# Kernel tuning notes

Hardware: AMD Instinct MI355X
Metric: run time of the kernel (lower is better)

The kernel has to match this reference:

```python
import jax, jax.numpy as jnp
import numpy as np

EMBED_DIM = 1024
HEAD_SIZE = 128
B, S = 8, 2048

def setup_inputs() -> dict:
    rng = jax.random.key(0)
    k1, k2, k3, k4, k5, k6 = jax.random.split(rng, 6)
    std = 1.0 / EMBED_DIM  # nn.initializers.normal(stddev=1/embed_dim)
    return {
        "key": jax.random.normal(k1, (B, S, EMBED_DIM), dtype=jnp.float32),
        "query": jax.random.normal(k2, (B, S, EMBED_DIM), dtype=jnp.float32),
        "value": jax.random.normal(k3, (B, S, EMBED_DIM), dtype=jnp.float32),
        "W_Q": jax.random.normal(k4, (EMBED_DIM, HEAD_SIZE), dtype=jnp.float32) * std,
        "W_K": jax.random.normal(k5, (EMBED_DIM, HEAD_SIZE), dtype=jnp.float32) * std,
        "W_V": jax.random.normal(k6, (EMBED_DIM, HEAD_SIZE), dtype=jnp.float32) * std,
    }

def reference(key, query, value, W_Q, W_K, W_V):
    # Parallel retention: (Q K^T * causal_mask) V
    q_proj = query @ W_Q        # (B, S, H)
    k_proj = key @ W_K          # (B, S, H)
    v_proj = value @ W_V        # (B, S, H)
    ret = jnp.einsum("bsh,bth->bst", q_proj, k_proj)  # (B, S, S)
    # full_self_retention=False -> lower-triangular (causal) mask
    decay_matrix = jnp.tril(jnp.ones((S, S), dtype=ret.dtype))
    ret = ret * decay_matrix
    return ret @ v_proj          # (B, S, H)
```

## Files before the change

### kernel.cpp

```cpp
#include <hip/hip_runtime.h>
#include <cstdint>

#define B_  8
#define S_  2048
#define E_  1024
#define H_  128
#define NC_ 16

typedef __attribute__((ext_vector_type(8))) short bf16x8;
typedef __attribute__((ext_vector_type(4))) float f32x4;

__device__ __forceinline__ short f2bf(float f){
  uint32_t u = __builtin_bit_cast(uint32_t, f);
  u = (u + 0x7fffu + ((u >> 16) & 1u)) >> 16;
  return (short)u;
}
__device__ __forceinline__ float bf2f(short s){
  uint32_t u = ((uint32_t)(uint16_t)s) << 16;
  return __builtin_bit_cast(float, u);
}
__device__ __forceinline__ void load_lds16(const void* g, void* l){
  __builtin_amdgcn_global_load_lds(
    (const __attribute__((address_space(1))) void*)g,
    (__attribute__((address_space(3))) void*)l, 16, 0, 0);
}

__global__ __launch_bounds__(256) void wt_kernel(
    const float* __restrict__ WQ, const float* __restrict__ WK,
    const float* __restrict__ WV,
    short* __restrict__ WtQ, short* __restrict__ WtK, short* __restrict__ WtV)
{
  int which = blockIdx.y;
  const float* W = which == 0 ? WQ : which == 1 ? WK : WV;
  short* Wt      = which == 0 ? WtQ : which == 1 ? WtK : WtV;
  int base = blockIdx.x * 4096;
  #pragma unroll
  for (int t = 0; t < 16; t++){
    int idx = base + t * 256 + threadIdx.x;
    int n  = idx >> 10;
    int kk = idx & 1023;
    Wt[idx] = f2bf(W[kk * H_ + n]);
  }
}

__global__ __launch_bounds__(256) void proj_kernel(
    const float* __restrict__ Xq, const float* __restrict__ Xk,
    const float* __restrict__ Xv,
    const short* __restrict__ Wtq, const short* __restrict__ Wtk,
    const short* __restrict__ Wtv,
    short* __restrict__ Pq, short* __restrict__ Pk, short* __restrict__ Pv)
{
  int which = blockIdx.y;
  const float* X  = which == 0 ? Xq  : which == 1 ? Xk  : Xv;
  const short* Wt = which == 0 ? Wtq : which == 1 ? Wtk : Wtv;
  short* P        = which == 0 ? Pq  : which == 1 ? Pk  : Pv;

  __shared__ float As[128 * 32];
  __shared__ short Bs[128 * 32];

  int tid  = threadIdx.x;
  int lane = tid & 63;
  int wave = tid >> 6;
  int wrow = (wave >> 1) * 64, wcol = (wave & 1) * 64;
  int lr = lane & 15, lq = lane >> 4;
  int row0 = blockIdx.x * 128;

  f32x4 acc[4][4];
  #pragma unroll
  for (int a = 0; a < 4; a++)
    #pragma unroll
    for (int c = 0; c < 4; c++) acc[a][c] = (f32x4){0.f, 0.f, 0.f, 0.f};

  for (int k0 = 0; k0 < E_; k0 += 32){
    __syncthreads();
    #pragma unroll
    for (int i = 0; i < 4; i++){
      int r = wave * 32 + i * 8 + (lane >> 3);
      int c = (lane & 7) * 4;
      load_lds16(X + (size_t)(row0 + r) * E_ + k0 + c,
                 (void*)(As + (wave * 32 + i * 8) * 32));
    }
    #pragma unroll
    for (int i = 0; i < 2; i++){
      int nr = wave * 32 + i * 16 + (lane >> 2);
      int c  = (lane & 3) * 8;
      load_lds16(Wt + (size_t)nr * E_ + k0 + c,
                 (void*)(Bs + (wave * 32 + i * 16) * 32));
    }
    __syncthreads();

    bf16x8 af[4], bf[4];
    #pragma unroll
    for (int tm = 0; tm < 4; tm++){
      const float* ap = As + (wrow + tm * 16 + lr) * 32 + lq * 8;
      f32x4 lo = *(const f32x4*)ap;
      f32x4 hi = *(const f32x4*)(ap + 4);
      bf16x8 a;
      #pragma unroll
      for (int j = 0; j < 4; j++){ a[j] = f2bf(lo[j]); a[4 + j] = f2bf(hi[j]); }
      af[tm] = a;
    }
    #pragma unroll
    for (int tn = 0; tn < 4; tn++)
      bf[tn] = *(const bf16x8*)(Bs + (wcol + tn * 16 + lr) * 32 + lq * 8);

    #pragma unroll
    for (int tm = 0; tm < 4; tm++)
      #pragma unroll
      for (int tn = 0; tn < 4; tn++)
        acc[tm][tn] = __builtin_amdgcn_mfma_f32_16x16x32_bf16(
            af[tm], bf[tn], acc[tm][tn], 0, 0, 0);
  }

  #pragma unroll
  for (int tm = 0; tm < 4; tm++)
    #pragma unroll
    for (int tn = 0; tn < 4; tn++)
      #pragma unroll
      for (int r4 = 0; r4 < 4; r4++){
        int row = row0 + wrow + tm * 16 + lq * 4 + r4;
        int col = wcol + tn * 16 + lr;
        P[(size_t)row * H_ + col] = f2bf(acc[tm][tn][r4]);
      }
}

__global__ __launch_bounds__(256) void transpose2(
    const short* __restrict__ k, const short* __restrict__ v,
    short* __restrict__ kT, short* __restrict__ vT)
{
  int b = blockIdx.z & 7;
  int which = blockIdx.z >> 3;
  const short* src = which ? v : k;
  short* dst       = which ? vT : kT;
  src += (size_t)b * S_ * H_;
  dst += (size_t)b * H_ * S_;
  int s0 = blockIdx.x * 32, h0 = blockIdx.y * 32;

  __shared__ short t[32][33];
  int tx = threadIdx.x & 31, ty = threadIdx.x >> 5;
  #pragma unroll
  for (int i = 0; i < 4; i++)
    t[ty + i * 8][tx] = src[(size_t)(s0 + ty + i * 8) * H_ + h0 + tx];
  __syncthreads();
  #pragma unroll
  for (int i = 0; i < 4; i++)
    dst[(size_t)(h0 + ty + i * 8) * S_ + s0 + tx] = t[tx][ty + i * 8];
}

__global__ __launch_bounds__(256) void chunk_state(
    const short* __restrict__ vT, const short* __restrict__ kT,
    float* __restrict__ M)
{
  int j = blockIdx.x, b = blockIdx.y;
  int tid = threadIdx.x, lane = tid & 63, wave = tid >> 6;
  int wrow = (wave >> 1) * 64, wcol = (wave & 1) * 64;
  int lr = lane & 15, lq = lane >> 4;

  __shared__ short As[128 * 32];
  __shared__ short Bs[128 * 32];

  const short* vtb = vT + (size_t)b * H_ * S_ + j * 128;
  const short* ktb = kT + (size_t)b * H_ * S_ + j * 128;

  f32x4 acc[4][4];
  #pragma unroll
  for (int a = 0; a < 4; a++)
    #pragma unroll
    for (int c = 0; c < 4; c++) acc[a][c] = (f32x4){0.f, 0.f, 0.f, 0.f};

  for (int t0 = 0; t0 < 128; t0 += 32){
    __syncthreads();
    #pragma unroll
    for (int i = 0; i < 2; i++){
      int r = wave * 32 + i * 16 + (lane >> 2);
      int c = (lane & 3) * 8;
      load_lds16(vtb + (size_t)r * S_ + t0 + c,
                 (void*)(As + (wave * 32 + i * 16) * 32));
      load_lds16(ktb + (size_t)r * S_ + t0 + c,
                 (void*)(Bs + (wave * 32 + i * 16) * 32));
    }
    __syncthreads();
    bf16x8 af[4], bf[4];
    #pragma unroll
    for (int tm = 0; tm < 4; tm++)
      af[tm] = *(const bf16x8*)(As + (wrow + tm * 16 + lr) * 32 + lq * 8);
    #pragma unroll
    for (int tn = 0; tn < 4; tn++)
      bf[tn] = *(const bf16x8*)(Bs + (wcol + tn * 16 + lr) * 32 + lq * 8);
    #pragma unroll
    for (int tm = 0; tm < 4; tm++)
      #pragma unroll
      for (int tn = 0; tn < 4; tn++)
        acc[tm][tn] = __builtin_amdgcn_mfma_f32_16x16x32_bf16(
            af[tm], bf[tn], acc[tm][tn], 0, 0, 0);
  }

  float* mb = M + (size_t)(b * NC_ + j) * 16384;
  #pragma unroll
  for (int tm = 0; tm < 4; tm++)
    #pragma unroll
    for (int tn = 0; tn < 4; tn++)
      #pragma unroll
      for (int r4 = 0; r4 < 4; r4++){
        int row = wrow + tm * 16 + lq * 4 + r4;
        int col = wcol + tn * 16 + lr;
        mb[row * 128 + col] = acc[tm][tn][r4];
      }
}

__global__ __launch_bounds__(256) void prefix_state(
    const float* __restrict__ M, short* __restrict__ Shi, short* __restrict__ Slo)
{
  int b = blockIdx.y;
  int idx = (blockIdx.x * 256 + threadIdx.x) * 4;
  float r0 = 0.f, r1 = 0.f, r2 = 0.f, r3 = 0.f;
  for (int j = 0; j < NC_; j++){
    size_t o = (size_t)(b * NC_ + j) * 16384 + idx;
    short h0 = f2bf(r0), h1 = f2bf(r1), h2 = f2bf(r2), h3 = f2bf(r3);
    short l0 = f2bf(r0 - bf2f(h0)), l1 = f2bf(r1 - bf2f(h1));
    short l2 = f2bf(r2 - bf2f(h2)), l3 = f2bf(r3 - bf2f(h3));
    union { short s[4]; uint2 u; } ph, pl;
    ph.s[0] = h0; ph.s[1] = h1; ph.s[2] = h2; ph.s[3] = h3;
    pl.s[0] = l0; pl.s[1] = l1; pl.s[2] = l2; pl.s[3] = l3;
    *(uint2*)(Shi + o) = ph.u;
    *(uint2*)(Slo + o) = pl.u;
    float4 mv = *(const float4*)(M + o);
    r0 += mv.x; r1 += mv.y; r2 += mv.z; r3 += mv.w;
  }
}

__global__ __launch_bounds__(256) void passC(
    const short* __restrict__ qb, const short* __restrict__ kb,
    const short* __restrict__ vT, const short* __restrict__ Shi,
    const short* __restrict__ Slo, float* __restrict__ out)
{
  int i = blockIdx.x, b = blockIdx.y;
  int tid = threadIdx.x, lane = tid & 63, wave = tid >> 6;
  int wrow = (wave >> 1) * 64, wcol = (wave & 1) * 64;
  int lr = lane & 15, lq = lane >> 4;

  __shared__ short Qs[128 * 136];
  __shared__ short Ss[128 * 136];
  __shared__ short Bsh[128 * 32];

  const short* qbase = qb + ((size_t)b * S_ + i * 128) * H_;
  const short* kbase = kb + ((size_t)b * S_ + i * 128) * H_;
  const short* vtb   = vT + (size_t)b * H_ * S_ + i * 128;
  const short* shib  = Shi + (size_t)(b * NC_ + i) * 16384;
  const short* slob  = Slo + (size_t)(b * NC_ + i) * 16384;

  #pragma unroll
  for (int t = 0; t < 8; t++){
    int chunk = t * 256 + tid;
    int s = chunk >> 4, c16 = chunk & 15;
    *(uint4*)(Qs + s * 136 + c16 * 8) =
        *(const uint4*)(qbase + s * H_ + c16 * 8);
  }

  f32x4 acc[4][4];
  #pragma unroll
  for (int a = 0; a < 4; a++)
    #pragma unroll
    for (int c = 0; c < 4; c++) acc[a][c] = (f32x4){0.f, 0.f, 0.f, 0.f};

  for (int h0 = 0; h0 < H_; h0 += 32){
    __syncthreads();
    #pragma unroll
    for (int t = 0; t < 2; t++){
      int r = wave * 32 + t * 16 + (lane >> 2);
      int c = (lane & 3) * 8;
      load_lds16(kbase + (size_t)r * H_ + h0 + c,
                 (void*)(Bsh + (wave * 32 + t * 16) * 32));
    }
    __syncthreads();
    bf16x8 af[4], bf[4];
    #pragma unroll
    for (int tm = 0; tm < 4; tm++)
      af[tm] = *(const bf16x8*)(Qs + (wrow + tm * 16 + lr) * 136 + h0 + lq * 8);
    #pragma unroll
    for (int tn = 0; tn < 4; tn++)
      bf[tn] = *(const bf16x8*)(Bsh + (wcol + tn * 16 + lr) * 32 + lq * 8);
    #pragma unroll
    for (int tm = 0; tm < 4; tm++)
      #pragma unroll
      for (int tn = 0; tn < 4; tn++)
        acc[tm][tn] = __builtin_amdgcn_mfma_f32_16x16x32_bf16(
            af[tm], bf[tn], acc[tm][tn], 0, 0, 0);
  }
  __syncthreads();

  #pragma unroll
  for (int tm = 0; tm < 4; tm++)
    #pragma unroll
    for (int tn = 0; tn < 4; tn++)
      #pragma unroll
      for (int r4 = 0; r4 < 4; r4++){
        int row = wrow + tm * 16 + lq * 4 + r4;
        int col = wcol + tn * 16 + lr;
        float vv = (col <= row) ? acc[tm][tn][r4] : 0.f;
        Ss[row * 136 + col] = f2bf(vv);
      }
  #pragma unroll
  for (int a = 0; a < 4; a++)
    #pragma unroll
    for (int c = 0; c < 4; c++) acc[a][c] = (f32x4){0.f, 0.f, 0.f, 0.f};
  __syncthreads();

  for (int t0 = 0; t0 < 128; t0 += 32){
    __syncthreads();
    #pragma unroll
    for (int t = 0; t < 2; t++){
      int r = wave * 32 + t * 16 + (lane >> 2);
      int c = (lane & 3) * 8;
      load_lds16(vtb + (size_t)r * S_ + t0 + c,
                 (void*)(Bsh + (wave * 32 + t * 16) * 32));
    }
    __syncthreads();
    bf16x8 af[4], bf[4];
    #pragma unroll
    for (int tm = 0; tm < 4; tm++)
      af[tm] = *(const bf16x8*)(Ss + (wrow + tm * 16 + lr) * 136 + t0 + lq * 8);
    #pragma unroll
    for (int tn = 0; tn < 4; tn++)
      bf[tn] = *(const bf16x8*)(Bsh + (wcol + tn * 16 + lr) * 32 + lq * 8);
    #pragma unroll
    for (int tm = 0; tm < 4; tm++)
      #pragma unroll
      for (int tn = 0; tn < 4; tn++)
        acc[tm][tn] = __builtin_amdgcn_mfma_f32_16x16x32_bf16(
            af[tm], bf[tn], acc[tm][tn], 0, 0, 0);
  }

  #pragma unroll
  for (int part = 0; part < 2; part++){
    const short* sb = part == 0 ? shib : slob;
    for (int h0 = 0; h0 < H_; h0 += 32){
      __syncthreads();
      #pragma unroll
      for (int t = 0; t < 2; t++){
        int r = wave * 32 + t * 16 + (lane >> 2);
        int c = (lane & 3) * 8;
        load_lds16(sb + (size_t)r * 128 + h0 + c,
                   (void*)(Bsh + (wave * 32 + t * 16) * 32));
      }
      __syncthreads();
      bf16x8 af[4], bf[4];
      #pragma unroll
      for (int tm = 0; tm < 4; tm++)
        af[tm] = *(const bf16x8*)(Qs + (wrow + tm * 16 + lr) * 136 + h0 + lq * 8);
      #pragma unroll
      for (int tn = 0; tn < 4; tn++)
        bf[tn] = *(const bf16x8*)(Bsh + (wcol + tn * 16 + lr) * 32 + lq * 8);
      #pragma unroll
      for (int tm = 0; tm < 4; tm++)
        #pragma unroll
        for (int tn = 0; tn < 4; tn++)
          acc[tm][tn] = __builtin_amdgcn_mfma_f32_16x16x32_bf16(
              af[tm], bf[tn], acc[tm][tn], 0, 0, 0);
    }
  }

  float* ob = out + ((size_t)b * S_ + i * 128) * H_;
  #pragma unroll
  for (int tm = 0; tm < 4; tm++)
    #pragma unroll
    for (int tn = 0; tn < 4; tn++)
      #pragma unroll
      for (int r4 = 0; r4 < 4; r4++){
        int row = wrow + tm * 16 + lq * 4 + r4;
        int col = wcol + tn * 16 + lr;
        ob[(size_t)row * H_ + col] = acc[tm][tn][r4];
      }
}

extern "C" void kernel_launch(void* const* d_in, const int* in_sizes, int n_in,
                              void* d_out, int out_size, void* d_ws, size_t ws_size,
                              hipStream_t stream) {
  const float* key   = (const float*)d_in[0];
  const float* query = (const float*)d_in[1];
  const float* value = (const float*)d_in[2];
  const float* WQ    = (const float*)d_in[3];
  const float* WK    = (const float*)d_in[4];
  const float* WV    = (const float*)d_in[5];
  float* out = (float*)d_out;

  char* w = (char*)d_ws;
  short* WtQ = (short*)(w + 0);
  short* WtK = (short*)(w + 262144);
  short* WtV = (short*)(w + 524288);
  size_t o = 786432;
  short* q  = (short*)(w + o); o += 4194304;
  short* k  = (short*)(w + o); o += 4194304;
  short* v  = (short*)(w + o); o += 4194304;
  short* kT = (short*)(w + o); o += 4194304;
  short* vT = (short*)(w + o); o += 4194304;
  float* M  = (float*)(w + o); o += 8388608;
  short* Shi= (short*)(w + o); o += 4194304;
  short* Slo= (short*)(w + o); o += 4194304;

  wt_kernel   <<<dim3(32, 3),          256, 0, stream>>>(WQ, WK, WV, WtQ, WtK, WtV);
  proj_kernel <<<dim3(128, 3),         256, 0, stream>>>(query, key, value,
                                                         WtQ, WtK, WtV, q, k, v);
  transpose2  <<<dim3(64, 4, 16),      256, 0, stream>>>(k, v, kT, vT);
  chunk_state <<<dim3(NC_, B_),        256, 0, stream>>>(vT, kT, M);
  prefix_state<<<dim3(16, B_),         256, 0, stream>>>(M, Shi, Slo);
  passC       <<<dim3(NC_, B_),        256, 0, stream>>>(q, k, vT, Shi, Slo, out);
}
```

Before: 244.9 us.

## Raise block counts in projection and output passes; tile weight transpose; batch prefix loads

```diff
diff --git a/kernel.cpp b/kernel.cpp
--- a/kernel.cpp
+++ b/kernel.cpp
@@ -30,17 +30,19 @@
     const float* __restrict__ WV,
     short* __restrict__ WtQ, short* __restrict__ WtK, short* __restrict__ WtV)
 {
-  int which = blockIdx.y;
+  int which = blockIdx.z;
   const float* W = which == 0 ? WQ : which == 1 ? WK : WV;
   short* Wt      = which == 0 ? WtQ : which == 1 ? WtK : WtV;
-  int base = blockIdx.x * 4096;
-  #pragma unroll
-  for (int t = 0; t < 16; t++){
-    int idx = base + t * 256 + threadIdx.x;
-    int n  = idx >> 10;
-    int kk = idx & 1023;
-    Wt[idx] = f2bf(W[kk * H_ + n]);
-  }
+  int k0 = blockIdx.x * 32, n0 = blockIdx.y * 32;
+  __shared__ float t[32][33];
+  int tx = threadIdx.x & 31, ty = threadIdx.x >> 5;
+  #pragma unroll
+  for (int i = 0; i < 4; i++)
+    t[ty + i * 8][tx] = W[(size_t)(k0 + ty + i * 8) * H_ + n0 + tx];
+  __syncthreads();
+  #pragma unroll
+  for (int i = 0; i < 4; i++)
+    Wt[(size_t)(n0 + ty + i * 8) * E_ + k0 + tx] = f2bf(t[tx][ty + i * 8]);
 }
 
 __global__ __launch_bounds__(256) void proj_kernel(
@@ -55,73 +57,52 @@
   const short* Wt = which == 0 ? Wtq : which == 1 ? Wtk : Wtv;
   short* P        = which == 0 ? Pq  : which == 1 ? Pk  : Pv;
 
-  __shared__ float As[128 * 32];
-  __shared__ short Bs[128 * 32];
-
-  int tid  = threadIdx.x;
-  int lane = tid & 63;
-  int wave = tid >> 6;
-  int wrow = (wave >> 1) * 64, wcol = (wave & 1) * 64;
+  int tid = threadIdx.x, lane = tid & 63, wave = tid >> 6;
   int lr = lane & 15, lq = lane >> 4;
-  int row0 = blockIdx.x * 128;
-
-  f32x4 acc[4][4];
-  #pragma unroll
-  for (int a = 0; a < 4; a++)
-    #pragma unroll
-    for (int c = 0; c < 4; c++) acc[a][c] = (f32x4){0.f, 0.f, 0.f, 0.f};
-
-  for (int k0 = 0; k0 < E_; k0 += 32){
-    __syncthreads();
-    #pragma unroll
-    for (int i = 0; i < 4; i++){
-      int r = wave * 32 + i * 8 + (lane >> 3);
-      int c = (lane & 7) * 4;
-      load_lds16(X + (size_t)(row0 + r) * E_ + k0 + c,
-                 (void*)(As + (wave * 32 + i * 8) * 32));
-    }
-    #pragma unroll
-    for (int i = 0; i < 2; i++){
-      int nr = wave * 32 + i * 16 + (lane >> 2);
-      int c  = (lane & 3) * 8;
-      load_lds16(Wt + (size_t)nr * E_ + k0 + c,
-                 (void*)(Bs + (wave * 32 + i * 16) * 32));
-    }
-    __syncthreads();
-
-    bf16x8 af[4], bf[4];
-    #pragma unroll
-    for (int tm = 0; tm < 4; tm++){
-      const float* ap = As + (wrow + tm * 16 + lr) * 32 + lq * 8;
-      f32x4 lo = *(const f32x4*)ap;
-      f32x4 hi = *(const f32x4*)(ap + 4);
-      bf16x8 a;
-      #pragma unroll
-      for (int j = 0; j < 4; j++){ a[j] = f2bf(lo[j]); a[4 + j] = f2bf(hi[j]); }
-      af[tm] = a;
-    }
-    #pragma unroll
-    for (int tn = 0; tn < 4; tn++)
-      bf[tn] = *(const bf16x8*)(Bs + (wcol + tn * 16 + lr) * 32 + lq * 8);
-
-    #pragma unroll
-    for (int tm = 0; tm < 4; tm++)
-      #pragma unroll
-      for (int tn = 0; tn < 4; tn++)
-        acc[tm][tn] = __builtin_amdgcn_mfma_f32_16x16x32_bf16(
-            af[tm], bf[tn], acc[tm][tn], 0, 0, 0);
-  }
-
-  #pragma unroll
-  for (int tm = 0; tm < 4; tm++)
-    #pragma unroll
-    for (int tn = 0; tn < 4; tn++)
-      #pragma unroll
-      for (int r4 = 0; r4 < 4; r4++){
-        int row = row0 + wrow + tm * 16 + lq * 4 + r4;
-        int col = wcol + tn * 16 + lr;
-        P[(size_t)row * H_ + col] = f2bf(acc[tm][tn][r4]);
-      }
+  int rowbase = blockIdx.x * 64 + wave * 16;
+
+  const float* xr = X + (size_t)(rowbase + lr) * E_ + lq * 8;
+  const short* wb = Wt + (size_t)lr * E_ + lq * 8;
+
+  f32x4 acc[8];
+  #pragma unroll
+  for (int tn = 0; tn < 8; tn++) acc[tn] = (f32x4){0.f, 0.f, 0.f, 0.f};
+
+  f32x4 alo = *(const f32x4*)xr;
+  f32x4 ahi = *(const f32x4*)(xr + 4);
+  bf16x8 bfr[8];
+  #pragma unroll
+  for (int tn = 0; tn < 8; tn++)
+    bfr[tn] = *(const bf16x8*)(wb + (size_t)tn * 16 * E_);
+
+  #pragma unroll 4
+  for (int k0 = 32; k0 <= E_; k0 += 32){
+    bf16x8 a;
+    #pragma unroll
+    for (int j = 0; j < 4; j++){ a[j] = f2bf(alo[j]); a[4 + j] = f2bf(ahi[j]); }
+    bf16x8 bc[8];
+    #pragma unroll
+    for (int tn = 0; tn < 8; tn++) bc[tn] = bfr[tn];
+    if (k0 < E_){
+      alo = *(const f32x4*)(xr + k0);
+      ahi = *(const f32x4*)(xr + k0 + 4);
+      #pragma unroll
+      for (int tn = 0; tn < 8; tn++)
+        bfr[tn] = *(const bf16x8*)(wb + (size_t)tn * 16 * E_ + k0);
+    }
+    #pragma unroll
+    for (int tn = 0; tn < 8; tn++)
+      acc[tn] = __builtin_amdgcn_mfma_f32_16x16x32_bf16(a, bc[tn], acc[tn], 0, 0, 0);
+  }
+
+  #pragma unroll
+  for (int tn = 0; tn < 8; tn++)
+    #pragma unroll
+    for (int r4 = 0; r4 < 4; r4++){
+      int row = rowbase + lq * 4 + r4;
+      int col = tn * 16 + lr;
+      P[(size_t)row * H_ + col] = f2bf(acc[tn][r4]);
+    }
 }
 
 __global__ __launch_bounds__(256) void transpose2(
@@ -213,7 +194,13 @@
 {
   int b = blockIdx.y;
   int idx = (blockIdx.x * 256 + threadIdx.x) * 4;
+  float4 mv[NC_];
+  #pragma unroll
+  for (int j = 0; j < NC_; j++)
+    mv[j] = *(const float4*)(M + (size_t)(b * NC_ + j) * 16384 + idx);
+
   float r0 = 0.f, r1 = 0.f, r2 = 0.f, r3 = 0.f;
+  #pragma unroll
   for (int j = 0; j < NC_; j++){
     size_t o = (size_t)(b * NC_ + j) * 16384 + idx;
     short h0 = f2bf(r0), h1 = f2bf(r1), h2 = f2bf(r2), h3 = f2bf(r3);
@@ -224,8 +211,7 @@
     pl.s[0] = l0; pl.s[1] = l1; pl.s[2] = l2; pl.s[3] = l3;
     *(uint2*)(Shi + o) = ph.u;
     *(uint2*)(Slo + o) = pl.u;
-    float4 mv = *(const float4*)(M + o);
-    r0 += mv.x; r1 += mv.y; r2 += mv.z; r3 += mv.w;
+    r0 += mv[j].x; r1 += mv[j].y; r2 += mv[j].z; r3 += mv[j].w;
   }
 }
 
@@ -234,32 +220,33 @@
     const short* __restrict__ vT, const short* __restrict__ Shi,
     const short* __restrict__ Slo, float* __restrict__ out)
 {
-  int i = blockIdx.x, b = blockIdx.y;
+  int i = blockIdx.x, half = blockIdx.y, b = blockIdx.z;
+  int roff = half * 64;
   int tid = threadIdx.x, lane = tid & 63, wave = tid >> 6;
-  int wrow = (wave >> 1) * 64, wcol = (wave & 1) * 64;
+  int wrow = (wave >> 1) * 32, wcol = (wave & 1) * 64;
   int lr = lane & 15, lq = lane >> 4;
 
-  __shared__ short Qs[128 * 136];
-  __shared__ short Ss[128 * 136];
+  __shared__ short Qs[64 * 136];
+  __shared__ short Ss[64 * 136];
   __shared__ short Bsh[128 * 32];
 
-  const short* qbase = qb + ((size_t)b * S_ + i * 128) * H_;
+  const short* qbase = qb + ((size_t)b * S_ + i * 128 + roff) * H_;
   const short* kbase = kb + ((size_t)b * S_ + i * 128) * H_;
   const short* vtb   = vT + (size_t)b * H_ * S_ + i * 128;
   const short* shib  = Shi + (size_t)(b * NC_ + i) * 16384;
   const short* slob  = Slo + (size_t)(b * NC_ + i) * 16384;
 
   #pragma unroll
-  for (int t = 0; t < 8; t++){
+  for (int t = 0; t < 4; t++){
     int chunk = t * 256 + tid;
     int s = chunk >> 4, c16 = chunk & 15;
     *(uint4*)(Qs + s * 136 + c16 * 8) =
         *(const uint4*)(qbase + s * H_ + c16 * 8);
   }
 
-  f32x4 acc[4][4];
-  #pragma unroll
-  for (int a = 0; a < 4; a++)
+  f32x4 acc[2][4];
+  #pragma unroll
+  for (int a = 0; a < 2; a++)
     #pragma unroll
     for (int c = 0; c < 4; c++) acc[a][c] = (f32x4){0.f, 0.f, 0.f, 0.f};
 
@@ -273,15 +260,15 @@
                  (void*)(Bsh + (wave * 32 + t * 16) * 32));
     }
     __syncthreads();
-    bf16x8 af[4], bf[4];
-    #pragma unroll
-    for (int tm = 0; tm < 4; tm++)
+    bf16x8 af[2], bf[4];
+    #pragma unroll
+    for (int tm = 0; tm < 2; tm++)
       af[tm] = *(const bf16x8*)(Qs + (wrow + tm * 16 + lr) * 136 + h0 + lq * 8);
     #pragma unroll
     for (int tn = 0; tn < 4; tn++)
       bf[tn] = *(const bf16x8*)(Bsh + (wcol + tn * 16 + lr) * 32 + lq * 8);
     #pragma unroll
-    for (int tm = 0; tm < 4; tm++)
+    for (int tm = 0; tm < 2; tm++)
       #pragma unroll
       for (int tn = 0; tn < 4; tn++)
         acc[tm][tn] = __builtin_amdgcn_mfma_f32_16x16x32_bf16(
@@ -290,18 +277,18 @@
   __syncthreads();
 
   #pragma unroll
-  for (int tm = 0; tm < 4; tm++)
+  for (int tm = 0; tm < 2; tm++)
     #pragma unroll
     for (int tn = 0; tn < 4; tn++)
       #pragma unroll
       for (int r4 = 0; r4 < 4; r4++){
         int row = wrow + tm * 16 + lq * 4 + r4;
         int col = wcol + tn * 16 + lr;
-        float vv = (col <= row) ? acc[tm][tn][r4] : 0.f;
+        float vv = (col <= roff + row) ? acc[tm][tn][r4] : 0.f;
         Ss[row * 136 + col] = f2bf(vv);
       }
   #pragma unroll
-  for (int a = 0; a < 4; a++)
+  for (int a = 0; a < 2; a++)
     #pragma unroll
     for (int c = 0; c < 4; c++) acc[a][c] = (f32x4){0.f, 0.f, 0.f, 0.f};
   __syncthreads();
@@ -316,15 +303,15 @@
                  (void*)(Bsh + (wave * 32 + t * 16) * 32));
     }
     __syncthreads();
-    bf16x8 af[4], bf[4];
-    #pragma unroll
-    for (int tm = 0; tm < 4; tm++)
+    bf16x8 af[2], bf[4];
+    #pragma unroll
+    for (int tm = 0; tm < 2; tm++)
       af[tm] = *(const bf16x8*)(Ss + (wrow + tm * 16 + lr) * 136 + t0 + lq * 8);
     #pragma unroll
     for (int tn = 0; tn < 4; tn++)
       bf[tn] = *(const bf16x8*)(Bsh + (wcol + tn * 16 + lr) * 32 + lq * 8);
     #pragma unroll
-    for (int tm = 0; tm < 4; tm++)
+    for (int tm = 0; tm < 2; tm++)
       #pragma unroll
       for (int tn = 0; tn < 4; tn++)
         acc[tm][tn] = __builtin_amdgcn_mfma_f32_16x16x32_bf16(
@@ -344,15 +331,15 @@
                    (void*)(Bsh + (wave * 32 + t * 16) * 32));
       }
       __syncthreads();
-      bf16x8 af[4], bf[4];
-      #pragma unroll
-      for (int tm = 0; tm < 4; tm++)
+      bf16x8 af[2], bf[4];
+      #pragma unroll
+      for (int tm = 0; tm < 2; tm++)
         af[tm] = *(const bf16x8*)(Qs + (wrow + tm * 16 + lr) * 136 + h0 + lq * 8);
       #pragma unroll
       for (int tn = 0; tn < 4; tn++)
         bf[tn] = *(const bf16x8*)(Bsh + (wcol + tn * 16 + lr) * 32 + lq * 8);
       #pragma unroll
-      for (int tm = 0; tm < 4; tm++)
+      for (int tm = 0; tm < 2; tm++)
         #pragma unroll
         for (int tn = 0; tn < 4; tn++)
           acc[tm][tn] = __builtin_amdgcn_mfma_f32_16x16x32_bf16(
@@ -360,9 +347,9 @@
     }
   }
 
-  float* ob = out + ((size_t)b * S_ + i * 128) * H_;
-  #pragma unroll
-  for (int tm = 0; tm < 4; tm++)
+  float* ob = out + ((size_t)b * S_ + i * 128 + roff) * H_;
+  #pragma unroll
+  for (int tm = 0; tm < 2; tm++)
     #pragma unroll
     for (int tn = 0; tn < 4; tn++)
       #pragma unroll
@@ -398,11 +385,11 @@
   short* Shi= (short*)(w + o); o += 4194304;
   short* Slo= (short*)(w + o); o += 4194304;
 
-  wt_kernel   <<<dim3(32, 3),          256, 0, stream>>>(WQ, WK, WV, WtQ, WtK, WtV);
-  proj_kernel <<<dim3(128, 3),         256, 0, stream>>>(query, key, value,
+  wt_kernel   <<<dim3(32, 4, 3),       256, 0, stream>>>(WQ, WK, WV, WtQ, WtK, WtV);
+  proj_kernel <<<dim3(256, 3),         256, 0, stream>>>(query, key, value,
                                                          WtQ, WtK, WtV, q, k, v);
   transpose2  <<<dim3(64, 4, 16),      256, 0, stream>>>(k, v, kT, vT);
   chunk_state <<<dim3(NC_, B_),        256, 0, stream>>>(vT, kT, M);
   prefix_state<<<dim3(16, B_),         256, 0, stream>>>(M, Shi, Slo);
-  passC       <<<dim3(NC_, B_),        256, 0, stream>>>(q, k, vT, Shi, Slo, out);
-}
+  passC       <<<dim3(NC_, 2, B_),     256, 0, stream>>>(q, k, vT, Shi, Slo, out);
+}
```

Measured after the change: 291.1 us. +18.9%, slower.
